# Kernel optimization log

Hardware: AMD Instinct MI355X
Metric: run time of the kernel (lower is better)

Reference implementation:

```python
import jax, jax.numpy as jnp
import numpy as np

B, L, N, D, C = 256, 512, 64, 32, 100  # batch, latent_dim, num_concepts, box_dim, num_classes


def setup_inputs() -> dict:
    key = jax.random.key(0)
    ks = jax.random.split(key, 11)
    s = 0.02  # weight init scale
    return {
        "h": jax.random.normal(ks[0], (B, L), dtype=jnp.float32),
        "Wc": jax.random.normal(ks[1], (N, L, D), dtype=jnp.float32) * s,
        "bc": jax.random.normal(ks[2], (N, D), dtype=jnp.float32) * s,
        "Wo": jax.random.normal(ks[3], (N, L, D), dtype=jnp.float32) * s,
        "bo": jax.random.normal(ks[4], (N, D), dtype=jnp.float32) * s,
        "Wp": jax.random.normal(ks[5], (N, 2 * D), dtype=jnp.float32) * s,
        "bp": jax.random.normal(ks[6], (N,), dtype=jnp.float32) * s,
        "W1": jax.random.normal(ks[7], (N * 2 * D, C), dtype=jnp.float32) * s,
        "b1": jax.random.normal(ks[8], (C,), dtype=jnp.float32) * s,
        "W2": jax.random.normal(ks[9], (N * N, C), dtype=jnp.float32) * s,
        "b2": jax.random.normal(ks[10], (C,), dtype=jnp.float32) * s,
    }


def reference(h, Wc, bc, Wo, bo, Wp, bp, W1, b1, W2, b2):
    EPS = 1e-6
    batch = h.shape[0]
    # Batched per-concept projections (replaces N un-batched Linears)
    x_m = jnp.einsum('bl,nld->bnd', h, Wc) + bc                    # [B,N,D] centers
    delta = jax.nn.softplus(jnp.einsum('bl,nld->bnd', h, Wo) + bo)  # [B,N,D] offsets
    box = jnp.concatenate([x_m, delta], axis=-1)                    # [B,N,2D]
    # Per-concept probability heads
    p_hat = jax.nn.sigmoid(jnp.einsum('bnd,nd->bn', box, Wp) + bp)  # [B,N]
    # Pairwise intersection volumes, fully broadcast (replaces N^2 loop)
    lo = x_m - delta  # [B,N,D]
    hi = x_m + delta
    inter = jnp.minimum(hi[:, :, None, :], hi[:, None, :, :]) - \
            jnp.maximum(lo[:, :, None, :], lo[:, None, :, :])       # [B,N,N,D]
    inter_off = jax.nn.relu(inter) * 0.5
    vol_inter = jnp.prod(inter_off + EPS, axis=-1)                  # [B,N,N]
    vol = jnp.prod(delta + EPS, axis=-1)                            # [B,N]
    V = vol_inter / vol[:, None, :]                                 # V[b,i,j] = |i∩j|/|j|
    # Classification heads
    aligned_flat = (box * p_hat[..., None]).reshape(batch, -1)      # [B, N*2D]
    y_hat = aligned_flat @ W1 + b1 + V.reshape(batch, -1) @ W2 + b2  # [B,C]
    return y_hat, p_hat, V
```

## Files before the change

### kernel.cpp

```cpp
#include <hip/hip_runtime.h>
#include <hip/hip_bf16.h>
#include <cstdint>

constexpr int Bb = 256, Ll = 512, Nn = 64, Dd = 32, Cc = 100;
constexpr float EPS = 1e-6f;

typedef __attribute__((ext_vector_type(8))) short short8;
typedef __attribute__((ext_vector_type(4))) float f32x4;

__device__ __forceinline__ unsigned short f2bf(float f) {
  union { float f; uint32_t u; } v; v.f = f;
  uint32_t r = v.u + 0x7FFFu + ((v.u >> 16) & 1u);
  return (unsigned short)(r >> 16);
}

__global__ __launch_bounds__(256) void kA(
    const float* __restrict__ h,
    const float* __restrict__ Wc,
    const float* __restrict__ bc,
    const float* __restrict__ Wo,
    const float* __restrict__ bo,
    const float* __restrict__ Wp,
    const float* __restrict__ bp,
    float* __restrict__ xm_ws,
    float* __restrict__ dl_ws,
    float* __restrict__ ph_ws,
    float* __restrict__ out_ph)
{
  const int n  = blockIdx.x;
  const int bt = blockIdx.y * 64;
  const int t  = threadIdx.x;
  const int w  = t >> 6, l = t & 63;
  const int lr = l & 15, lg = l >> 4;

  __shared__ unsigned short hb[64][64];
  __shared__ unsigned short wbT[64][72];

  f32x4 acc[4] = {};

  const int hr = t >> 2,        hc = (t & 3) * 16;
  const int wk = (t >> 3) * 2,  wcq = (t & 7) * 4;
  const float* hsrc  = h  + (bt + hr) * Ll + hc;
  const float* wcsrc = Wc + n * (Ll * Dd) + wk * Dd + wcq;
  const float* wosrc = Wo + n * (Ll * Dd) + wk * Dd + wcq;

  float4 hp0, hp1, hp2, hp3, c0, c1, o0, o1;
  auto fetch = [&](int k0) {
    const float* hs = hsrc + k0;
    hp0 = *(const float4*)(hs);
    hp1 = *(const float4*)(hs + 4);
    hp2 = *(const float4*)(hs + 8);
    hp3 = *(const float4*)(hs + 12);
    const float* ws = wcsrc + k0 * Dd;
    c0 = *(const float4*)(ws);
    c1 = *(const float4*)(ws + Dd);
    const float* os = wosrc + k0 * Dd;
    o0 = *(const float4*)(os);
    o1 = *(const float4*)(os + Dd);
  };

  fetch(0);
  for (int ch = 0; ch < 8; ch++) {
    __syncthreads();
    {
      unsigned short* hd = &hb[hr][hc];
      hd[0]  = f2bf(hp0.x); hd[1]  = f2bf(hp0.y);
      hd[2]  = f2bf(hp0.z); hd[3]  = f2bf(hp0.w);
      hd[4]  = f2bf(hp1.x); hd[5]  = f2bf(hp1.y);
      hd[6]  = f2bf(hp1.z); hd[7]  = f2bf(hp1.w);
      hd[8]  = f2bf(hp2.x); hd[9]  = f2bf(hp2.y);
      hd[10] = f2bf(hp2.z); hd[11] = f2bf(hp2.w);
      hd[12] = f2bf(hp3.x); hd[13] = f2bf(hp3.y);
      hd[14] = f2bf(hp3.z); hd[15] = f2bf(hp3.w);
    }
    {
      const float* c0p = &c0.x; const float* c1p = &c1.x;
      const float* o0p = &o0.x; const float* o1p = &o1.x;
      #pragma unroll
      for (int i = 0; i < 4; i++) {
        unsigned int pc = (unsigned int)f2bf(c0p[i]) |
                          ((unsigned int)f2bf(c1p[i]) << 16);
        *(unsigned int*)&wbT[wcq + i][wk] = pc;
        unsigned int po = (unsigned int)f2bf(o0p[i]) |
                          ((unsigned int)f2bf(o1p[i]) << 16);
        *(unsigned int*)&wbT[32 + wcq + i][wk] = po;
      }
    }
    __syncthreads();
    if (ch < 7) fetch((ch + 1) * 64);
    const int arow = w * 16 + lr;
    #pragma unroll
    for (int ks = 0; ks < 2; ks++) {
      const int ko = ks * 32 + lg * 8;
      const short8 av = *(const short8*)&hb[arow][ko];
      #pragma unroll
      for (int nf = 0; nf < 4; nf++) {
        const short8 bv = *(const short8*)&wbT[nf * 16 + lr][ko];
        acc[nf] = __builtin_amdgcn_mfma_f32_16x16x32_bf16(av, bv, acc[nf],
                                                          0, 0, 0);
      }
    }
  }

  const float bc0 = bc[n * Dd + lr],      bc1 = bc[n * Dd + 16 + lr];
  const float bo0 = bo[n * Dd + lr],      bo1 = bo[n * Dd + 16 + lr];
  const float wp0 = Wp[n * 64 + lr],      wp1 = Wp[n * 64 + 16 + lr];
  const float wp2 = Wp[n * 64 + 32 + lr], wp3 = Wp[n * 64 + 48 + lr];
  const float bpv = bp[n];

  #pragma unroll
  for (int q = 0; q < 4; q++) {
    const int b = bt + w * 16 + lg * 4 + q;
    const float xm0  = acc[0][q] + bc0;
    const float xm1  = acc[1][q] + bc1;
    const float pre0 = acc[2][q] + bo0;
    const float pre1 = acc[3][q] + bo1;
    const float dl0 = fmaxf(pre0, 0.f) + log1pf(expf(-fabsf(pre0)));
    const float dl1 = fmaxf(pre1, 0.f) + log1pf(expf(-fabsf(pre1)));
    float* xp = xm_ws + b * 2048 + n * Dd;
    float* dp = dl_ws + b * 2048 + n * Dd;
    xp[lr] = xm0;  xp[16 + lr] = xm1;
    dp[lr] = dl0;  dp[16 + lr] = dl1;
    float pp = xm0 * wp0 + xm1 * wp1 + dl0 * wp2 + dl1 * wp3;
    pp += __shfl_xor(pp, 1);
    pp += __shfl_xor(pp, 2);
    pp += __shfl_xor(pp, 4);
    pp += __shfl_xor(pp, 8);
    if (lr == 0) {
      const float ph = 1.f / (1.f + expf(-(pp + bpv)));
      ph_ws[b * 64 + n] = ph;
      out_ph[b * 64 + n] = ph;
    }
  }
}

__global__ __launch_bounds__(256) void kB(
    const float* __restrict__ xm_ws,
    const float* __restrict__ dl_ws,
    float* __restrict__ out_V)
{
  const int b = blockIdx.x, t = threadIdx.x;
  __shared__ float lo[64][36];
  __shared__ float hi[64][36];
  __shared__ float rvol[64];

  {
    const int n = t >> 2, dd = (t & 3) * 8;
    const float* xp = xm_ws + b * 2048 + n * Dd + dd;
    const float* dp = dl_ws + b * 2048 + n * Dd + dd;
    #pragma unroll
    for (int i = 0; i < 8; i += 4) {
      float4 x = *(const float4*)(xp + i);
      float4 g = *(const float4*)(dp + i);
      lo[n][dd + i + 0] = x.x - g.x;  hi[n][dd + i + 0] = x.x + g.x;
      lo[n][dd + i + 1] = x.y - g.y;  hi[n][dd + i + 1] = x.y + g.y;
      lo[n][dd + i + 2] = x.z - g.z;  hi[n][dd + i + 2] = x.z + g.z;
      lo[n][dd + i + 3] = x.w - g.w;  hi[n][dd + i + 3] = x.w + g.w;
    }
  }
  if (t < 64) {
    const float* dp = dl_ws + b * 2048 + t * Dd;
    float p = 1.f;
    #pragma unroll
    for (int dd = 0; dd < 32; dd++) p *= dp[dd] + EPS;
    rvol[t] = 1.f / p;
  }
  __syncthreads();

  const int i0 = t >> 6;
  const int j  = t & 63;
  #pragma unroll 1
  for (int it = 0; it < 16; it++) {
    const int i = i0 + 4 * it;
    float prod = 1.f;
    #pragma unroll
    for (int dd = 0; dd < 32; dd += 4) {
      float4 hj = *(const float4*)&hi[j][dd];
      float4 lj = *(const float4*)&lo[j][dd];
      float4 hv = *(const float4*)&hi[i][dd];
      float4 lv = *(const float4*)&lo[i][dd];
      float v0 = fmaxf(fminf(hv.x, hj.x) - fmaxf(lv.x, lj.x), 0.f) * 0.5f + EPS;
      float v1 = fmaxf(fminf(hv.y, hj.y) - fmaxf(lv.y, lj.y), 0.f) * 0.5f + EPS;
      float v2 = fmaxf(fminf(hv.z, hj.z) - fmaxf(lv.z, lj.z), 0.f) * 0.5f + EPS;
      float v3 = fmaxf(fminf(hv.w, hj.w) - fmaxf(lv.w, lj.w), 0.f) * 0.5f + EPS;
      prod *= v0 * v1 * v2 * v3;
    }
    out_V[b * 4096 + i * 64 + j] = prod * rvol[j];
  }
}

__global__ __launch_bounds__(256) void kC1(
    const float* __restrict__ xm_ws,
    const float* __restrict__ dl_ws,
    const float* __restrict__ ph_ws,
    const float* __restrict__ Vb,
    const float* __restrict__ W1,
    const float* __restrict__ W2,
    float* __restrict__ part)
{
  const int bg = blockIdx.x;
  const int s  = blockIdx.y;
  const bool isV = (s >= 16);
  const int m0 = (s & 15) * 256;
  const float* __restrict__ W = isV ? W2 : W1;

  __shared__ float Wt[64][132];
  __shared__ float At[64][33];

  const int t  = threadIdx.x;
  const int tx = t & 15;
  const int ty = t >> 4;

  float acc[2][8] = {};

  const int wrw = t >> 2, wq8 = (t & 3) * 8;
  const int arow = t >> 3, agk = t & 7;
  const int brow_s = bg * 32 + arow;

  float4 wreg[8];
  float4 a0, a1;
  auto load_chunk = [&](int mbase) {
    const float* wr = W + (mbase + wrw) * Cc;
    #pragma unroll
    for (int j = 0; j < 8; j++) {
      const int c = (wq8 + j) * 4;
      wreg[j] = (c < Cc) ? *(const float4*)(wr + c)
                         : make_float4(0.f, 0.f, 0.f, 0.f);
    }
    const int mk = mbase + agk * 8;
    if (!isV) {
      const int nn = mk >> 6, sub = mk & 63;
      const float phv = ph_ws[brow_s * 64 + nn];
      const float* src = (sub < 32)
          ? (xm_ws + brow_s * 2048 + nn * Dd + sub)
          : (dl_ws + brow_s * 2048 + nn * Dd + (sub - 32));
      a0 = *(const float4*)(src);
      a1 = *(const float4*)(src + 4);
      a0.x *= phv; a0.y *= phv; a0.z *= phv; a0.w *= phv;
      a1.x *= phv; a1.y *= phv; a1.z *= phv; a1.w *= phv;
    } else {
      const float* src = Vb + brow_s * 4096 + mk;
      a0 = *(const float4*)(src);
      a1 = *(const float4*)(src + 4);
    }
  };

  load_chunk(m0);
  for (int ch = 0; ch < 4; ch++) {
    __syncthreads();
    #pragma unroll
    for (int j = 0; j < 8; j++) {
      const int c = (wq8 + j) * 4;
      if (c < Cc) *(float4*)&Wt[wrw][c] = wreg[j];
    }
    {
      const int k8 = agk * 8;
      At[k8 + 0][arow] = a0.x; At[k8 + 1][arow] = a0.y;
      At[k8 + 2][arow] = a0.z; At[k8 + 3][arow] = a0.w;
      At[k8 + 4][arow] = a1.x; At[k8 + 5][arow] = a1.y;
      At[k8 + 6][arow] = a1.z; At[k8 + 7][arow] = a1.w;
    }
    __syncthreads();
    if (ch < 3) load_chunk(m0 + (ch + 1) * 64);
    #pragma unroll 8
    for (int kk = 0; kk < 64; kk++) {
      const float av0 = At[kk][ty * 2];
      const float av1 = At[kk][ty * 2 + 1];
      float4 wlo = *(const float4*)&Wt[kk][tx * 4];
      float4 whi = *(const float4*)&Wt[kk][(tx + 16) * 4];
      acc[0][0] += av0 * wlo.x; acc[0][1] += av0 * wlo.y;
      acc[0][2] += av0 * wlo.z; acc[0][3] += av0 * wlo.w;
      acc[0][4] += av0 * whi.x; acc[0][5] += av0 * whi.y;
      acc[0][6] += av0 * whi.z; acc[0][7] += av0 * whi.w;
      acc[1][0] += av1 * wlo.x; acc[1][1] += av1 * wlo.y;
      acc[1][2] += av1 * wlo.z; acc[1][3] += av1 * wlo.w;
      acc[1][4] += av1 * whi.x; acc[1][5] += av1 * whi.y;
      acc[1][6] += av1 * whi.z; acc[1][7] += av1 * whi.w;
    }
  }

  #pragma unroll
  for (int r = 0; r < 2; r++) {
    const int brow = bg * 32 + ty * 2 + r;
    float* pr = part + (s * 256 + brow) * Cc;
    #pragma unroll
    for (int q = 0; q < 2; q++) {
      const int c0 = (tx + q * 16) * 4;
      if (c0 < Cc) {
        pr[c0 + 0] = acc[r][q * 4 + 0];
        pr[c0 + 1] = acc[r][q * 4 + 1];
        pr[c0 + 2] = acc[r][q * 4 + 2];
        pr[c0 + 3] = acc[r][q * 4 + 3];
      }
    }
  }
}

__global__ __launch_bounds__(256) void kC2(
    const float* __restrict__ part,
    const float* __restrict__ b1,
    const float* __restrict__ b2,
    float* __restrict__ out_y)
{
  const int o = blockIdx.x * 256 + threadIdx.x;
  const int c = o % Cc;
  float sum = b1[c] + b2[c];
  #pragma unroll
  for (int s = 0; s < 32; s++) sum += part[s * 25600 + o];
  out_y[o] = sum;
}

extern "C" void kernel_launch(void* const* d_in, const int* in_sizes, int n_in,
                              void* d_out, int out_size, void* d_ws, size_t ws_size,
                              hipStream_t stream) {
  const float* h  = (const float*)d_in[0];
  const float* Wc = (const float*)d_in[1];
  const float* bc = (const float*)d_in[2];
  const float* Wo = (const float*)d_in[3];
  const float* bo = (const float*)d_in[4];
  const float* Wp = (const float*)d_in[5];
  const float* bp = (const float*)d_in[6];
  const float* W1 = (const float*)d_in[7];
  const float* b1 = (const float*)d_in[8];
  const float* W2 = (const float*)d_in[9];
  const float* b2 = (const float*)d_in[10];

  float* out    = (float*)d_out;
  float* out_y  = out;
  float* out_ph = out + Bb * Cc;
  float* out_V  = out + Bb * Cc + Bb * Nn;

  float* xm   = (float*)d_ws;
  float* dl   = xm + Bb * Nn * Dd;
  float* ph   = dl + Bb * Nn * Dd;
  float* part = ph + Bb * Nn;

  kA<<<dim3(Nn, Bb / 64), 256, 0, stream>>>(h, Wc, bc, Wo, bo, Wp, bp,
                                            xm, dl, ph, out_ph);
  kB<<<Bb, 256, 0, stream>>>(xm, dl, out_V);
  kC1<<<dim3(8, 32), 256, 0, stream>>>(xm, dl, ph, (const float*)out_V,
                                       W1, W2, part);
  kC2<<<100, 256, 0, stream>>>(part, b1, b2, out_y);
}
```

Before: 52.73 us.

## Fuse four kernels into one cooperative persistent kernel with grid syncs

```diff
diff --git a/kernel.cpp b/kernel.cpp
--- a/kernel.cpp
+++ b/kernel.cpp
@@ -1,6 +1,9 @@
 #include <hip/hip_runtime.h>
+#include <hip/hip_cooperative_groups.h>
 #include <hip/hip_bf16.h>
 #include <cstdint>
+
+namespace cg = cooperative_groups;
 
 constexpr int Bb = 256, Ll = 512, Nn = 64, Dd = 32, Cc = 100;
 constexpr float EPS = 1e-6f;
@@ -14,7 +17,23 @@
   return (unsigned short)(r >> 16);
 }
 
-__global__ __launch_bounds__(256) void kA(
+union USm {
+  struct {
+    unsigned short hb[64][64];
+    unsigned short wbT[64][72];
+  } a;
+  struct {
+    float lo[64][36];
+    float hi[64][36];
+    float rvol[64];
+  } b;
+  struct {
+    float Wt[64][132];
+    float At[64][68];
+  } c;
+};
+
+__global__ __launch_bounds__(256) void fused(
     const float* __restrict__ h,
     const float* __restrict__ Wc,
     const float* __restrict__ bc,
@@ -22,292 +41,292 @@
     const float* __restrict__ bo,
     const float* __restrict__ Wp,
     const float* __restrict__ bp,
+    const float* __restrict__ W1,
+    const float* __restrict__ b1,
+    const float* __restrict__ W2,
+    const float* __restrict__ b2,
     float* __restrict__ xm_ws,
     float* __restrict__ dl_ws,
     float* __restrict__ ph_ws,
-    float* __restrict__ out_ph)
-{
-  const int n  = blockIdx.x;
-  const int bt = blockIdx.y * 64;
-  const int t  = threadIdx.x;
-  const int w  = t >> 6, l = t & 63;
-  const int lr = l & 15, lg = l >> 4;
-
-  __shared__ unsigned short hb[64][64];
-  __shared__ unsigned short wbT[64][72];
-
-  f32x4 acc[4] = {};
-
-  const int hr = t >> 2,        hc = (t & 3) * 16;
-  const int wk = (t >> 3) * 2,  wcq = (t & 7) * 4;
-  const float* hsrc  = h  + (bt + hr) * Ll + hc;
-  const float* wcsrc = Wc + n * (Ll * Dd) + wk * Dd + wcq;
-  const float* wosrc = Wo + n * (Ll * Dd) + wk * Dd + wcq;
-
-  float4 hp0, hp1, hp2, hp3, c0, c1, o0, o1;
-  auto fetch = [&](int k0) {
-    const float* hs = hsrc + k0;
-    hp0 = *(const float4*)(hs);
-    hp1 = *(const float4*)(hs + 4);
-    hp2 = *(const float4*)(hs + 8);
-    hp3 = *(const float4*)(hs + 12);
-    const float* ws = wcsrc + k0 * Dd;
-    c0 = *(const float4*)(ws);
-    c1 = *(const float4*)(ws + Dd);
-    const float* os = wosrc + k0 * Dd;
-    o0 = *(const float4*)(os);
-    o1 = *(const float4*)(os + Dd);
-  };
-
-  fetch(0);
-  for (int ch = 0; ch < 8; ch++) {
-    __syncthreads();
-    {
-      unsigned short* hd = &hb[hr][hc];
-      hd[0]  = f2bf(hp0.x); hd[1]  = f2bf(hp0.y);
-      hd[2]  = f2bf(hp0.z); hd[3]  = f2bf(hp0.w);
-      hd[4]  = f2bf(hp1.x); hd[5]  = f2bf(hp1.y);
-      hd[6]  = f2bf(hp1.z); hd[7]  = f2bf(hp1.w);
-      hd[8]  = f2bf(hp2.x); hd[9]  = f2bf(hp2.y);
-      hd[10] = f2bf(hp2.z); hd[11] = f2bf(hp2.w);
-      hd[12] = f2bf(hp3.x); hd[13] = f2bf(hp3.y);
-      hd[14] = f2bf(hp3.z); hd[15] = f2bf(hp3.w);
-    }
-    {
-      const float* c0p = &c0.x; const float* c1p = &c1.x;
-      const float* o0p = &o0.x; const float* o1p = &o1.x;
-      #pragma unroll
-      for (int i = 0; i < 4; i++) {
-        unsigned int pc = (unsigned int)f2bf(c0p[i]) |
-                          ((unsigned int)f2bf(c1p[i]) << 16);
-        *(unsigned int*)&wbT[wcq + i][wk] = pc;
-        unsigned int po = (unsigned int)f2bf(o0p[i]) |
-                          ((unsigned int)f2bf(o1p[i]) << 16);
-        *(unsigned int*)&wbT[32 + wcq + i][wk] = po;
-      }
-    }
-    __syncthreads();
-    if (ch < 7) fetch((ch + 1) * 64);
-    const int arow = w * 16 + lr;
-    #pragma unroll
-    for (int ks = 0; ks < 2; ks++) {
-      const int ko = ks * 32 + lg * 8;
-      const short8 av = *(const short8*)&hb[arow][ko];
-      #pragma unroll
-      for (int nf = 0; nf < 4; nf++) {
-        const short8 bv = *(const short8*)&wbT[nf * 16 + lr][ko];
-        acc[nf] = __builtin_amdgcn_mfma_f32_16x16x32_bf16(av, bv, acc[nf],
-                                                          0, 0, 0);
-      }
-    }
-  }
-
-  const float bc0 = bc[n * Dd + lr],      bc1 = bc[n * Dd + 16 + lr];
-  const float bo0 = bo[n * Dd + lr],      bo1 = bo[n * Dd + 16 + lr];
-  const float wp0 = Wp[n * 64 + lr],      wp1 = Wp[n * 64 + 16 + lr];
-  const float wp2 = Wp[n * 64 + 32 + lr], wp3 = Wp[n * 64 + 48 + lr];
-  const float bpv = bp[n];
-
-  #pragma unroll
-  for (int q = 0; q < 4; q++) {
-    const int b = bt + w * 16 + lg * 4 + q;
-    const float xm0  = acc[0][q] + bc0;
-    const float xm1  = acc[1][q] + bc1;
-    const float pre0 = acc[2][q] + bo0;
-    const float pre1 = acc[3][q] + bo1;
-    const float dl0 = fmaxf(pre0, 0.f) + log1pf(expf(-fabsf(pre0)));
-    const float dl1 = fmaxf(pre1, 0.f) + log1pf(expf(-fabsf(pre1)));
-    float* xp = xm_ws + b * 2048 + n * Dd;
-    float* dp = dl_ws + b * 2048 + n * Dd;
-    xp[lr] = xm0;  xp[16 + lr] = xm1;
-    dp[lr] = dl0;  dp[16 + lr] = dl1;
-    float pp = xm0 * wp0 + xm1 * wp1 + dl0 * wp2 + dl1 * wp3;
-    pp += __shfl_xor(pp, 1);
-    pp += __shfl_xor(pp, 2);
-    pp += __shfl_xor(pp, 4);
-    pp += __shfl_xor(pp, 8);
-    if (lr == 0) {
-      const float ph = 1.f / (1.f + expf(-(pp + bpv)));
-      ph_ws[b * 64 + n] = ph;
-      out_ph[b * 64 + n] = ph;
-    }
-  }
-}
-
-__global__ __launch_bounds__(256) void kB(
-    const float* __restrict__ xm_ws,
-    const float* __restrict__ dl_ws,
+    float* __restrict__ part,
+    float* __restrict__ out_y,
+    float* __restrict__ out_ph,
     float* __restrict__ out_V)
 {
-  const int b = blockIdx.x, t = threadIdx.x;
-  __shared__ float lo[64][36];
-  __shared__ float hi[64][36];
-  __shared__ float rvol[64];
+  __shared__ USm u;
+  cg::grid_group grid = cg::this_grid();
+  const int bid = blockIdx.x;
+  const int t   = threadIdx.x;
 
   {
-    const int n = t >> 2, dd = (t & 3) * 8;
-    const float* xp = xm_ws + b * 2048 + n * Dd + dd;
-    const float* dp = dl_ws + b * 2048 + n * Dd + dd;
+    const int n  = bid & 63;
+    const int bt = (bid >> 6) * 64;
+    const int w  = t >> 6, l = t & 63;
+    const int lr = l & 15, lg = l >> 4;
+
+    f32x4 acc[4] = {};
+
+    const int hr = t >> 2,       hc  = (t & 3) * 16;
+    const int wk = (t >> 3) * 2, wcq = (t & 7) * 4;
+    const float* hsrc  = h  + (bt + hr) * Ll + hc;
+    const float* wcsrc = Wc + n * (Ll * Dd) + wk * Dd + wcq;
+    const float* wosrc = Wo + n * (Ll * Dd) + wk * Dd + wcq;
+
+    float4 hp0, hp1, hp2, hp3, c0, c1, o0, o1;
+    auto fetch = [&](int k0) {
+      const float* hs = hsrc + k0;
+      hp0 = *(const float4*)(hs);
+      hp1 = *(const float4*)(hs + 4);
+      hp2 = *(const float4*)(hs + 8);
+      hp3 = *(const float4*)(hs + 12);
+      const float* ws = wcsrc + k0 * Dd;
+      c0 = *(const float4*)(ws);
+      c1 = *(const float4*)(ws + Dd);
+      const float* os = wosrc + k0 * Dd;
+      o0 = *(const float4*)(os);
+      o1 = *(const float4*)(os + Dd);
+    };
+
+    fetch(0);
+    for (int ch = 0; ch < 8; ch++) {
+      __syncthreads();
+      {
+        unsigned short* hd = &u.a.hb[hr][hc];
+        hd[0]  = f2bf(hp0.x); hd[1]  = f2bf(hp0.y);
+        hd[2]  = f2bf(hp0.z); hd[3]  = f2bf(hp0.w);
+        hd[4]  = f2bf(hp1.x); hd[5]  = f2bf(hp1.y);
+        hd[6]  = f2bf(hp1.z); hd[7]  = f2bf(hp1.w);
+        hd[8]  = f2bf(hp2.x); hd[9]  = f2bf(hp2.y);
+        hd[10] = f2bf(hp2.z); hd[11] = f2bf(hp2.w);
+        hd[12] = f2bf(hp3.x); hd[13] = f2bf(hp3.y);
+        hd[14] = f2bf(hp3.z); hd[15] = f2bf(hp3.w);
+      }
+      {
+        const float* c0p = &c0.x; const float* c1p = &c1.x;
+        const float* o0p = &o0.x; const float* o1p = &o1.x;
+        #pragma unroll
+        for (int i = 0; i < 4; i++) {
+          unsigned int pc = (unsigned int)f2bf(c0p[i]) |
+                            ((unsigned int)f2bf(c1p[i]) << 16);
+          *(unsigned int*)&u.a.wbT[wcq + i][wk] = pc;
+          unsigned int po = (unsigned int)f2bf(o0p[i]) |
+                            ((unsigned int)f2bf(o1p[i]) << 16);
+          *(unsigned int*)&u.a.wbT[32 + wcq + i][wk] = po;
+        }
+      }
+      __syncthreads();
+      if (ch < 7) fetch((ch + 1) * 64);
+      const int arow = w * 16 + lr;
+      #pragma unroll
+      for (int ks = 0; ks < 2; ks++) {
+        const int ko = ks * 32 + lg * 8;
+        const short8 av = *(const short8*)&u.a.hb[arow][ko];
+        #pragma unroll
+        for (int nf = 0; nf < 4; nf++) {
+          const short8 bv = *(const short8*)&u.a.wbT[nf * 16 + lr][ko];
+          acc[nf] = __builtin_amdgcn_mfma_f32_16x16x32_bf16(av, bv, acc[nf],
+                                                            0, 0, 0);
+        }
+      }
+    }
+
+    const float bc0 = bc[n * Dd + lr],      bc1 = bc[n * Dd + 16 + lr];
+    const float bo0 = bo[n * Dd + lr],      bo1 = bo[n * Dd + 16 + lr];
+    const float wp0 = Wp[n * 64 + lr],      wp1 = Wp[n * 64 + 16 + lr];
+    const float wp2 = Wp[n * 64 + 32 + lr], wp3 = Wp[n * 64 + 48 + lr];
+    const float bpv = bp[n];
+
     #pragma unroll
-    for (int i = 0; i < 8; i += 4) {
-      float4 x = *(const float4*)(xp + i);
-      float4 g = *(const float4*)(dp + i);
-      lo[n][dd + i + 0] = x.x - g.x;  hi[n][dd + i + 0] = x.x + g.x;
-      lo[n][dd + i + 1] = x.y - g.y;  hi[n][dd + i + 1] = x.y + g.y;
-      lo[n][dd + i + 2] = x.z - g.z;  hi[n][dd + i + 2] = x.z + g.z;
-      lo[n][dd + i + 3] = x.w - g.w;  hi[n][dd + i + 3] = x.w + g.w;
+    for (int q = 0; q < 4; q++) {
+      const int b = bt + w * 16 + lg * 4 + q;
+      const float xm0  = acc[0][q] + bc0;
+      const float xm1  = acc[1][q] + bc1;
+      const float pre0 = acc[2][q] + bo0;
+      const float pre1 = acc[3][q] + bo1;
+      const float dl0 = fmaxf(pre0, 0.f) + log1pf(expf(-fabsf(pre0)));
+      const float dl1 = fmaxf(pre1, 0.f) + log1pf(expf(-fabsf(pre1)));
+      float* xp = xm_ws + b * 2048 + n * Dd;
+      float* dp = dl_ws + b * 2048 + n * Dd;
+      xp[lr] = xm0;  xp[16 + lr] = xm1;
+      dp[lr] = dl0;  dp[16 + lr] = dl1;
+      float pp = xm0 * wp0 + xm1 * wp1 + dl0 * wp2 + dl1 * wp3;
+      pp += __shfl_xor(pp, 1);
+      pp += __shfl_xor(pp, 2);
+      pp += __shfl_xor(pp, 4);
+      pp += __shfl_xor(pp, 8);
+      if (lr == 0) {
+        const float ph = 1.f / (1.f + expf(-(pp + bpv)));
+        ph_ws[b * 64 + n] = ph;
+        out_ph[b * 64 + n] = ph;
+      }
     }
   }
-  if (t < 64) {
-    const float* dp = dl_ws + b * 2048 + t * Dd;
-    float p = 1.f;
+  grid.sync();
+
+  {
+    const int b = bid;
+    {
+      const int n = t >> 2, dd = (t & 3) * 8;
+      const float* xp = xm_ws + b * 2048 + n * Dd + dd;
+      const float* dp = dl_ws + b * 2048 + n * Dd + dd;
+      #pragma unroll
+      for (int i = 0; i < 8; i += 4) {
+        float4 x = *(const float4*)(xp + i);
+        float4 g = *(const float4*)(dp + i);
+        u.b.lo[n][dd + i + 0] = x.x - g.x;  u.b.hi[n][dd + i + 0] = x.x + g.x;
+        u.b.lo[n][dd + i + 1] = x.y - g.y;  u.b.hi[n][dd + i + 1] = x.y + g.y;
+        u.b.lo[n][dd + i + 2] = x.z - g.z;  u.b.hi[n][dd + i + 2] = x.z + g.z;
+        u.b.lo[n][dd + i + 3] = x.w - g.w;  u.b.hi[n][dd + i + 3] = x.w + g.w;
+      }
+    }
+    if (t < 64) {
+      const float* dp = dl_ws + b * 2048 + t * Dd;
+      float p = 1.f;
+      #pragma unroll
+      for (int dd = 0; dd < 32; dd++) p *= dp[dd] + EPS;
+      u.b.rvol[t] = 1.f / p;
+    }
+    __syncthreads();
+
+    const int i0 = t >> 6;
+    const int j  = t & 63;
+    #pragma unroll 1
+    for (int it = 0; it < 16; it++) {
+      const int i = i0 + 4 * it;
+      float prod = 1.f;
+      #pragma unroll
+      for (int dd = 0; dd < 32; dd += 4) {
+        float4 hj = *(const float4*)&u.b.hi[j][dd];
+        float4 lj = *(const float4*)&u.b.lo[j][dd];
+        float4 hv = *(const float4*)&u.b.hi[i][dd];
+        float4 lv = *(const float4*)&u.b.lo[i][dd];
+        float v0 = fmaxf(fminf(hv.x,hj.x)-fmaxf(lv.x,lj.x),0.f)*0.5f + EPS;
+        float v1 = fmaxf(fminf(hv.y,hj.y)-fmaxf(lv.y,lj.y),0.f)*0.5f + EPS;
+        float v2 = fmaxf(fminf(hv.z,hj.z)-fmaxf(lv.z,lj.z),0.f)*0.5f + EPS;
+        float v3 = fmaxf(fminf(hv.w,hj.w)-fmaxf(lv.w,lj.w),0.f)*0.5f + EPS;
+        prod *= v0 * v1 * v2 * v3;
+      }
+      out_V[b * 4096 + i * 64 + j] = prod * u.b.rvol[j];
+    }
+    __syncthreads();
+  }
+  grid.sync();
+
+  {
+    const int bg = bid & 3;
+    const int s  = bid >> 2;
+    const bool isV = (s >= 32);
+    const int m0 = (s & 31) * 128;
+    const float* __restrict__ W = isV ? W2 : W1;
+
+    const int tx = t & 15;
+    const int ty = t >> 4;
+
+    float acc[4][8] = {};
+
+    const int wrw = t >> 2, wq8 = (t & 3) * 8;
+    const int arow = t >> 2, aq = t & 3;
+    const int brow_s = bg * 64 + arow;
+
+    float4 wreg[8];
+    float4 areg[2][2];
+    auto load_chunk = [&](int mbase) {
+      const float* wr = W + (mbase + wrw) * Cc;
+      #pragma unroll
+      for (int j = 0; j < 8; j++) {
+        const int c = (wq8 + j) * 4;
+        wreg[j] = (c < Cc) ? *(const float4*)(wr + c)
+                           : make_float4(0.f, 0.f, 0.f, 0.f);
+      }
+      #pragma unroll
+      for (int p = 0; p < 2; p++) {
+        const int mk = mbase + (aq + p * 4) * 8;
+        if (!isV) {
+          const int nn = mk >> 6, sub = mk & 63;
+          const float phv = ph_ws[brow_s * 64 + nn];
+          const float* src = (sub < 32)
+              ? (xm_ws + brow_s * 2048 + nn * Dd + sub)
+              : (dl_ws + brow_s * 2048 + nn * Dd + (sub - 32));
+          float4 v0 = *(const float4*)(src);
+          float4 v1 = *(const float4*)(src + 4);
+          v0.x *= phv; v0.y *= phv; v0.z *= phv; v0.w *= phv;
+          v1.x *= phv; v1.y *= phv; v1.z *= phv; v1.w *= phv;
+          areg[p][0] = v0; areg[p][1] = v1;
+        } else {
+          const float* src = out_V + brow_s * 4096 + mk;
+          areg[p][0] = *(const float4*)(src);
+          areg[p][1] = *(const float4*)(src + 4);
+        }
+      }
+    };
+
+    load_chunk(m0);
+    for (int ch = 0; ch < 2; ch++) {
+      __syncthreads();
+      #pragma unroll
+      for (int j = 0; j < 8; j++) {
+        const int c = (wq8 + j) * 4;
+        if (c < Cc) *(float4*)&u.c.Wt[wrw][c] = wreg[j];
+      }
+      #pragma unroll
+      for (int p = 0; p < 2; p++) {
+        const int k8 = (aq + p * 4) * 8;
+        u.c.At[k8 + 0][arow] = areg[p][0].x;
+        u.c.At[k8 + 1][arow] = areg[p][0].y;
+        u.c.At[k8 + 2][arow] = areg[p][0].z;
+        u.c.At[k8 + 3][arow] = areg[p][0].w;
+        u.c.At[k8 + 4][arow] = areg[p][1].x;
+        u.c.At[k8 + 5][arow] = areg[p][1].y;
+        u.c.At[k8 + 6][arow] = areg[p][1].z;
+        u.c.At[k8 + 7][arow] = areg[p][1].w;
+      }
+      __syncthreads();
+      if (ch == 0) load_chunk(m0 + 64);
+      #pragma unroll 4
+      for (int kk = 0; kk < 64; kk++) {
+        const float4 a4  = *(const float4*)&u.c.At[kk][ty * 4];
+        const float4 wlo = *(const float4*)&u.c.Wt[kk][tx * 4];
+        const float4 whi = *(const float4*)&u.c.Wt[kk][(tx + 16) * 4];
+        const float* ap = &a4.x;
+        #pragma unroll
+        for (int r = 0; r < 4; r++) {
+          const float av = ap[r];
+          acc[r][0] += av * wlo.x; acc[r][1] += av * wlo.y;
+          acc[r][2] += av * wlo.z; acc[r][3] += av * wlo.w;
+          acc[r][4] += av * whi.x; acc[r][5] += av * whi.y;
+          acc[r][6] += av * whi.z; acc[r][7] += av * whi.w;
+        }
+      }
+    }
+
     #pragma unroll
-    for (int dd = 0; dd < 32; dd++) p *= dp[dd] + EPS;
-    rvol[t] = 1.f / p;
+    for (int r = 0; r < 4; r++) {
+      const int brow = bg * 64 + ty * 4 + r;
+      float* pr = part + (s * 256 + brow) * Cc;
+      #pragma unroll
+      for (int q = 0; q < 2; q++) {
+        const int c0 = (tx + q * 16) * 4;
+        if (c0 < Cc) {
+          pr[c0 + 0] = acc[r][q * 4 + 0];
+          pr[c0 + 1] = acc[r][q * 4 + 1];
+          pr[c0 + 2] = acc[r][q * 4 + 2];
+          pr[c0 + 3] = acc[r][q * 4 + 3];
+        }
+      }
+    }
   }
-  __syncthreads();
-
-  const int i0 = t >> 6;
-  const int j  = t & 63;
-  #pragma unroll 1
-  for (int it = 0; it < 16; it++) {
-    const int i = i0 + 4 * it;
-    float prod = 1.f;
-    #pragma unroll
-    for (int dd = 0; dd < 32; dd += 4) {
-      float4 hj = *(const float4*)&hi[j][dd];
-      float4 lj = *(const float4*)&lo[j][dd];
-      float4 hv = *(const float4*)&hi[i][dd];
-      float4 lv = *(const float4*)&lo[i][dd];
-      float v0 = fmaxf(fminf(hv.x, hj.x) - fmaxf(lv.x, lj.x), 0.f) * 0.5f + EPS;
-      float v1 = fmaxf(fminf(hv.y, hj.y) - fmaxf(lv.y, lj.y), 0.f) * 0.5f + EPS;
-      float v2 = fmaxf(fminf(hv.z, hj.z) - fmaxf(lv.z, lj.z), 0.f) * 0.5f + EPS;
-      float v3 = fmaxf(fminf(hv.w, hj.w) - fmaxf(lv.w, lj.w), 0.f) * 0.5f + EPS;
-      prod *= v0 * v1 * v2 * v3;
-    }
-    out_V[b * 4096 + i * 64 + j] = prod * rvol[j];
+  grid.sync();
+
+  {
+    const int o = bid * 256 + t;
+    if (o < Bb * Cc) {
+      const int c = o % Cc;
+      float sum = b1[c] + b2[c];
+      #pragma unroll 8
+      for (int sl = 0; sl < 64; sl++) sum += part[sl * (Bb * Cc) + o];
+      out_y[o] = sum;
+    }
   }
-}
-
-__global__ __launch_bounds__(256) void kC1(
-    const float* __restrict__ xm_ws,
-    const float* __restrict__ dl_ws,
-    const float* __restrict__ ph_ws,
-    const float* __restrict__ Vb,
-    const float* __restrict__ W1,
-    const float* __restrict__ W2,
-    float* __restrict__ part)
-{
-  const int bg = blockIdx.x;
-  const int s  = blockIdx.y;
-  const bool isV = (s >= 16);
-  const int m0 = (s & 15) * 256;
-  const float* __restrict__ W = isV ? W2 : W1;
-
-  __shared__ float Wt[64][132];
-  __shared__ float At[64][33];
-
-  const int t  = threadIdx.x;
-  const int tx = t & 15;
-  const int ty = t >> 4;
-
-  float acc[2][8] = {};
-
-  const int wrw = t >> 2, wq8 = (t & 3) * 8;
-  const int arow = t >> 3, agk = t & 7;
-  const int brow_s = bg * 32 + arow;
-
-  float4 wreg[8];
-  float4 a0, a1;
-  auto load_chunk = [&](int mbase) {
-    const float* wr = W + (mbase + wrw) * Cc;
-    #pragma unroll
-    for (int j = 0; j < 8; j++) {
-      const int c = (wq8 + j) * 4;
-      wreg[j] = (c < Cc) ? *(const float4*)(wr + c)
-                         : make_float4(0.f, 0.f, 0.f, 0.f);
-    }
-    const int mk = mbase + agk * 8;
-    if (!isV) {
-      const int nn = mk >> 6, sub = mk & 63;
-      const float phv = ph_ws[brow_s * 64 + nn];
-      const float* src = (sub < 32)
-          ? (xm_ws + brow_s * 2048 + nn * Dd + sub)
-          : (dl_ws + brow_s * 2048 + nn * Dd + (sub - 32));
-      a0 = *(const float4*)(src);
-      a1 = *(const float4*)(src + 4);
-      a0.x *= phv; a0.y *= phv; a0.z *= phv; a0.w *= phv;
-      a1.x *= phv; a1.y *= phv; a1.z *= phv; a1.w *= phv;
-    } else {
-      const float* src = Vb + brow_s * 4096 + mk;
-      a0 = *(const float4*)(src);
-      a1 = *(const float4*)(src + 4);
-    }
-  };
-
-  load_chunk(m0);
-  for (int ch = 0; ch < 4; ch++) {
-    __syncthreads();
-    #pragma unroll
-    for (int j = 0; j < 8; j++) {
-      const int c = (wq8 + j) * 4;
-      if (c < Cc) *(float4*)&Wt[wrw][c] = wreg[j];
-    }
-    {
-      const int k8 = agk * 8;
-      At[k8 + 0][arow] = a0.x; At[k8 + 1][arow] = a0.y;
-      At[k8 + 2][arow] = a0.z; At[k8 + 3][arow] = a0.w;
-      At[k8 + 4][arow] = a1.x; At[k8 + 5][arow] = a1.y;
-      At[k8 + 6][arow] = a1.z; At[k8 + 7][arow] = a1.w;
-    }
-    __syncthreads();
-    if (ch < 3) load_chunk(m0 + (ch + 1) * 64);
-    #pragma unroll 8
-    for (int kk = 0; kk < 64; kk++) {
-      const float av0 = At[kk][ty * 2];
-      const float av1 = At[kk][ty * 2 + 1];
-      float4 wlo = *(const float4*)&Wt[kk][tx * 4];
-      float4 whi = *(const float4*)&Wt[kk][(tx + 16) * 4];
-      acc[0][0] += av0 * wlo.x; acc[0][1] += av0 * wlo.y;
-      acc[0][2] += av0 * wlo.z; acc[0][3] += av0 * wlo.w;
-      acc[0][4] += av0 * whi.x; acc[0][5] += av0 * whi.y;
-      acc[0][6] += av0 * whi.z; acc[0][7] += av0 * whi.w;
-      acc[1][0] += av1 * wlo.x; acc[1][1] += av1 * wlo.y;
-      acc[1][2] += av1 * wlo.z; acc[1][3] += av1 * wlo.w;
-      acc[1][4] += av1 * whi.x; acc[1][5] += av1 * whi.y;
-      acc[1][6] += av1 * whi.z; acc[1][7] += av1 * whi.w;
-    }
-  }
-
-  #pragma unroll
-  for (int r = 0; r < 2; r++) {
-    const int brow = bg * 32 + ty * 2 + r;
-    float* pr = part + (s * 256 + brow) * Cc;
-    #pragma unroll
-    for (int q = 0; q < 2; q++) {
-      const int c0 = (tx + q * 16) * 4;
-      if (c0 < Cc) {
-        pr[c0 + 0] = acc[r][q * 4 + 0];
-        pr[c0 + 1] = acc[r][q * 4 + 1];
-        pr[c0 + 2] = acc[r][q * 4 + 2];
-        pr[c0 + 3] = acc[r][q * 4 + 3];
-      }
-    }
-  }
-}
-
-__global__ __launch_bounds__(256) void kC2(
-    const float* __restrict__ part,
-    const float* __restrict__ b1,
-    const float* __restrict__ b2,
-    float* __restrict__ out_y)
-{
-  const int o = blockIdx.x * 256 + threadIdx.x;
-  const int c = o % Cc;
-  float sum = b1[c] + b2[c];
-  #pragma unroll
-  for (int s = 0; s < 32; s++) sum += part[s * 25600 + o];
-  out_y[o] = sum;
 }
 
 extern "C" void kernel_launch(void* const* d_in, const int* in_sizes, int n_in,
@@ -335,10 +354,12 @@
   float* ph   = dl + Bb * Nn * Dd;
   float* part = ph + Bb * Nn;
 
-  kA<<<dim3(Nn, Bb / 64), 256, 0, stream>>>(h, Wc, bc, Wo, bo, Wp, bp,
-                                            xm, dl, ph, out_ph);
-  kB<<<Bb, 256, 0, stream>>>(xm, dl, out_V);
-  kC1<<<dim3(8, 32), 256, 0, stream>>>(xm, dl, ph, (const float*)out_V,
-                                       W1, W2, part);
-  kC2<<<100, 256, 0, stream>>>(part, b1, b2, out_y);
+  void* args[] = {
+    (void*)&h,  (void*)&Wc, (void*)&bc, (void*)&Wo, (void*)&bo,
+    (void*)&Wp, (void*)&bp, (void*)&W1, (void*)&b1, (void*)&W2, (void*)&b2,
+    (void*)&xm, (void*)&dl, (void*)&ph, (void*)&part,
+    (void*)&out_y, (void*)&out_ph, (void*)&out_V
+  };
+  hipLaunchCooperativeKernel((const void*)fused, dim3(256), dim3(256),
+                             args, 0, stream);
 }
```

Result: slower. 146.1 us (+177.1%).
